# Kernel optimization log

Hardware: AMD Instinct MI355X
Metric: run time of the kernel (lower is better)

Reference implementation:

```python
import jax, jax.numpy as jnp
import numpy as np

_SAMPLING_EPS = 1e-5


def setup_inputs() -> dict:
    key = jax.random.key(0)
    k1, k2, k3, k4, k5 = jax.random.split(key, 5)
    B, V = 128, 128000
    logits = jax.random.normal(k1, (B, V), dtype=jnp.float32)
    temperature = jax.random.uniform(k2, (B,), dtype=jnp.float32)  # some rows < eps -> greedy
    top_k = jax.random.randint(k3, (B,), 1, 64, dtype=jnp.int32)   # in [1, 63]
    top_p = jax.random.uniform(k4, (B,), dtype=jnp.float32, minval=0.05, maxval=1.0)
    noise_u = jax.random.uniform(k5, (B, V), dtype=jnp.float32, minval=1e-10, maxval=1.0)
    return {"logits": logits, "temperature": temperature, "top_k": top_k,
            "top_p": top_p, "noise_u": noise_u, "max_num_logprobs": 5}


def _apply_top_k_top_p(logits, k, p):
    # Faithful to vLLM: ascending sort, top-k threshold mask, top-p cumsum mask, scatter back.
    B, V = logits.shape
    order = jnp.argsort(logits, axis=-1)                       # ascending, [B, V]
    logits_sort = jnp.take_along_axis(logits, order, axis=-1)
    neg_inf = jnp.float32(-jnp.inf)
    # top-k: pivot value at position V - k; everything strictly below it -> -inf
    pivot_idx = (V - k.astype(jnp.int32))[:, None]             # [B, 1]
    pivot = jnp.take_along_axis(logits_sort, pivot_idx, axis=-1)
    logits_sort = jnp.where(logits_sort < pivot, neg_inf, logits_sort)
    # top-p: softmax over sorted logits, cumsum, drop prefix with mass <= 1 - p (keep last)
    probs_sort = jax.nn.softmax(logits_sort, axis=-1)
    probs_sum = jnp.cumsum(probs_sort, axis=-1)
    top_p_mask = probs_sum <= (1.0 - p)[:, None]
    top_p_mask = top_p_mask.at[:, -1].set(False)
    logits_sort = jnp.where(top_p_mask, neg_inf, logits_sort)
    # scatter back to original vocab order
    rows = jnp.arange(B)[:, None]
    return jnp.zeros_like(logits).at[rows, order].set(logits_sort)


def reference(logits, temperature, top_k, top_p, noise_u, max_num_logprobs):
    # temperature scaling (temp < eps means greedy; divide by 1.0 instead)
    temp = jnp.where(temperature < _SAMPLING_EPS, 1.0, temperature)
    logits = logits.astype(jnp.float32) / temp[:, None]
    # top-k / top-p filtering
    logits = _apply_top_k_top_p(logits, top_k, top_p)
    # probabilities and sampling
    probs = jax.nn.softmax(logits, axis=-1)
    greedy = jnp.argmax(probs, axis=-1)
    q = -jnp.log(noise_u)                                      # Exp(1) noise (q.exponential_())
    random = jnp.argmax(probs / q, axis=-1)
    sampled = jnp.where(temperature < _SAMPLING_EPS, greedy, random).astype(jnp.int32)
    # top-k logprobs
    logprobs = jax.nn.log_softmax(logits, axis=-1)
    topk_logprobs, topk_indices = jax.lax.top_k(logprobs, max_num_logprobs)
    return sampled, topk_indices.astype(jnp.int32), topk_logprobs
```

## Files before the change

### kernel.cpp

```cpp
#include <hip/hip_runtime.h>
#include <math.h>
#include <stdint.h>

#define BT     256
#define TOPC   64
#define CAP    2048
#define WT     512
#define TILE   (BT * 8)
#define NCH    8
#define NC     (NCH * TOPC)

__device__ __forceinline__ unsigned f2ord(float f) {
    unsigned u = __float_as_uint(f);
    return u ^ ((u & 0x80000000u) ? 0xFFFFFFFFu : 0x80000000u);
}
__device__ __forceinline__ float ord2f(unsigned k) {
    unsigned u = (k & 0x80000000u) ? (k ^ 0x80000000u) : (k ^ 0xFFFFFFFFu);
    return __uint_as_float(u);
}

__device__ unsigned radix_select_compact4(uint2* s_buf, uint2* s_keep,
                                          unsigned (*s_hist)[16], unsigned* p_cnt2,
                                          unsigned n, int tid, int wid)
{
    unsigned prefix = 0u;
    int remaining = TOPC;
    for (int shift = 28; shift >= 0; shift -= 4) {
        if (tid < 64) ((unsigned*)s_hist)[tid] = 0u;
        __syncthreads();
        for (unsigned i = (unsigned)tid; i < n; i += BT) {
            unsigned k = s_buf[i].x;
            bool ing = (shift == 28) || ((k >> (shift + 4)) == (prefix >> (shift + 4)));
            if (ing) atomicAdd(&s_hist[wid][(k >> shift) & 15u], 1u);
        }
        __syncthreads();
        int cum = 0; int b = 0; unsigned hb = 0u;
        for (int bb = 15; bb >= 0; --bb) {
            unsigned h = s_hist[0][bb] + s_hist[1][bb] + s_hist[2][bb] + s_hist[3][bb];
            cum += (int)h;
            if (cum >= remaining) { b = bb; hb = h; break; }
        }
        remaining -= (cum - (int)hb);
        prefix |= ((unsigned)b) << shift;
        __syncthreads();
    }
    if (tid == 0) *p_cnt2 = 0u;
    __syncthreads();
    for (unsigned i = (unsigned)tid; i < n; i += BT) {
        uint2 c = s_buf[i];
        if (c.x > prefix) s_keep[atomicAdd(p_cnt2, 1u)] = c;
    }
    __syncthreads();
    for (unsigned i = (unsigned)tid; i < n; i += BT) {
        uint2 c = s_buf[i];
        if (c.x == prefix) {
            unsigned pos = atomicAdd(p_cnt2, 1u);
            if (pos < TOPC) s_keep[pos] = c;
        }
    }
    __syncthreads();
    return prefix;
}

__global__ __launch_bounds__(BT) void phase1_topk_chunks(
    const float* __restrict__ logits, uint2* __restrict__ cand,
    int V, int chunk_len, int nchunk)
{
    __shared__ uint2    s_buf[CAP];
    __shared__ uint2    s_keep[TOPC];
    __shared__ unsigned s_hist[4][16];
    __shared__ unsigned s_cnt, s_cnt2, s_ovf;

    const int row   = blockIdx.y;
    const int chunk = blockIdx.x;
    const int tid   = threadIdx.x;
    const int wid   = tid >> 6;
    const int lane  = tid & 63;
    const int c0    = chunk * chunk_len;
    int c1 = c0 + chunk_len; if (c1 > V) c1 = V;
    const float* rowp = logits + (size_t)row * (size_t)V;

    if (tid == 0) { s_cnt = 0u; s_ovf = 0u; }
    __syncthreads();

    const int slice_len = chunk_len >> 2;
    const int s0 = c0 + wid * slice_len;
    int s_end = s0 + slice_len; if (s_end > c1) s_end = c1;

    unsigned k0[8], k1[8];
    const int  b0  = s0 + lane * 8,  b1 = s0 + WT + lane * 8;
    const bool vv0 = (b0 < s_end),   vv1 = (b1 < s_end);
    if (vv0) {
        float4 a = *(const float4*)(rowp + b0);
        float4 b = *(const float4*)(rowp + b0 + 4);
        k0[0] = f2ord(a.x); k0[1] = f2ord(a.y); k0[2] = f2ord(a.z); k0[3] = f2ord(a.w);
        k0[4] = f2ord(b.x); k0[5] = f2ord(b.y); k0[6] = f2ord(b.z); k0[7] = f2ord(b.w);
    } else {
        #pragma unroll
        for (int j = 0; j < 8; ++j) k0[j] = 0u;
    }
    if (vv1) {
        float4 a = *(const float4*)(rowp + b1);
        float4 b = *(const float4*)(rowp + b1 + 4);
        k1[0] = f2ord(a.x); k1[1] = f2ord(a.y); k1[2] = f2ord(a.z); k1[3] = f2ord(a.w);
        k1[4] = f2ord(b.x); k1[5] = f2ord(b.y); k1[6] = f2ord(b.z); k1[7] = f2ord(b.w);
    } else {
        #pragma unroll
        for (int j = 0; j < 8; ++j) k1[j] = 0u;
    }

    float4 A0 = {}, B0 = {}, A1 = {}, B1 = {};
    bool v0 = false, v1 = false;
    const int t2 = s0 + 2 * WT, t3 = s0 + 3 * WT;
    if (t2 < s_end) {
        int bs = t2 + lane * 8;
        if (bs < s_end) { A0 = *(const float4*)(rowp + bs);
                          B0 = *(const float4*)(rowp + bs + 4); v0 = true; }
    }
    if (t3 < s_end) {
        int bs = t3 + lane * 8;
        if (bs < s_end) { A1 = *(const float4*)(rowp + bs);
                          B1 = *(const float4*)(rowp + bs + 4); v1 = true; }
    }

    unsigned lo = 0u, hi = 0xFFFFu;
    while (lo < hi) {
        unsigned mid = (lo + hi + 1u) >> 1;
        unsigned t = mid << 16;
        int cnt = 0;
        #pragma unroll
        for (int j = 0; j < 8; ++j) {
            cnt += __popcll(__ballot(k0[j] >= t));
            cnt += __popcll(__ballot(k1[j] >= t));
        }
        if (cnt >= TOPC) lo = mid; else hi = mid - 1u;
    }
    const unsigned thr = lo << 16;

    auto append8 = [&](const unsigned* k, int base, bool valid) {
        unsigned pm = 0u; unsigned np = 0u;
        if (valid) {
            #pragma unroll
            for (int j = 0; j < 8; ++j)
                if (k[j] >= thr) { pm |= (1u << j); ++np; }
        }
        if (np) {
            unsigned pos = atomicAdd(&s_cnt, np);
            #pragma unroll
            for (int j = 0; j < 8; ++j)
                if (pm & (1u << j)) {
                    if (pos < CAP) s_buf[pos] = make_uint2(k[j], (unsigned)(base + j));
                    ++pos;
                }
        }
    };

    append8(k0, b0, vv0);
    append8(k1, b1, vv1);

    for (int t = t2; t < s_end; t += WT) {
        float4 A2 = {}, B2 = {}; bool v2 = false;
        int tn = t + 2 * WT;
        if (tn < s_end) {
            int bs = tn + lane * 8;
            if (bs < s_end) { A2 = *(const float4*)(rowp + bs);
                              B2 = *(const float4*)(rowp + bs + 4); v2 = true; }
        }
        if (v0) {
            unsigned k[8];
            k[0] = f2ord(A0.x); k[1] = f2ord(A0.y); k[2] = f2ord(A0.z); k[3] = f2ord(A0.w);
            k[4] = f2ord(B0.x); k[5] = f2ord(B0.y); k[6] = f2ord(B0.z); k[7] = f2ord(B0.w);
            append8(k, t + lane * 8, true);
        }
        A0 = A1; B0 = B1; v0 = v1;
        A1 = A2; B1 = B2; v1 = v2;
    }

    __syncthreads();
    unsigned n = s_cnt;

    if (n > CAP) {
        unsigned vst = radix_select_compact4(s_buf, s_keep, s_hist, &s_cnt2,
                                             CAP, tid, wid);
        if (tid == 0) { s_cnt = 0u; s_ovf = 0u; }
        __syncthreads();
        for (int t = c0; t < c1; t += TILE) {
            int bs = t + tid * 8;
            unsigned k[8]; bool v = (bs < c1);
            if (v) {
                float4 a = *(const float4*)(rowp + bs);
                float4 b = *(const float4*)(rowp + bs + 4);
                k[0] = f2ord(a.x); k[1] = f2ord(a.y); k[2] = f2ord(a.z); k[3] = f2ord(a.w);
                k[4] = f2ord(b.x); k[5] = f2ord(b.y); k[6] = f2ord(b.z); k[7] = f2ord(b.w);
            } else {
                #pragma unroll
                for (int j = 0; j < 8; ++j) k[j] = 0u;
            }
            unsigned pm = 0u; int np = 0;
            if (v) {
                #pragma unroll
                for (int j = 0; j < 8; ++j)
                    if (k[j] >= vst) { pm |= (1u << j); ++np; }
            }
            for (;;) {
                if (np) {
                    unsigned pos = atomicAdd(&s_cnt, (unsigned)np);
                    unsigned rem = 0u; int nr = 0;
                    #pragma unroll
                    for (int j = 0; j < 8; ++j) {
                        if (pm & (1u << j)) {
                            if (pos < CAP) s_buf[pos] = make_uint2(k[j], (unsigned)(bs + j));
                            else { rem |= (1u << j); ++nr; }
                            ++pos;
                        }
                    }
                    if (nr) s_ovf = 1u;
                    pm = rem; np = nr;
                }
                __syncthreads();
                unsigned ovf = s_ovf;
                __syncthreads();
                if (!ovf) break;
                unsigned nn = s_cnt; if (nn > CAP) nn = CAP;
                unsigned v2s = radix_select_compact4(s_buf, s_keep, s_hist, &s_cnt2,
                                                     nn, tid, wid);
                if (tid < TOPC) s_buf[tid] = s_keep[tid];
                if (tid == 0) { s_cnt = TOPC; s_ovf = 0u; }
                __syncthreads();
                unsigned rem = 0u; int nr = 0;
                #pragma unroll
                for (int j = 0; j < 8; ++j)
                    if ((pm & (1u << j)) && k[j] > v2s) { rem |= (1u << j); ++nr; }
                pm = rem; np = nr;
            }
        }
        n = s_cnt; if (n > CAP) n = CAP;
    }

    if (n < TOPC) {
        for (unsigned i = n + (unsigned)tid; i < TOPC; i += BT)
            s_buf[i] = make_uint2(0u, (unsigned)((c0 < V) ? c0 : 0));
        n = TOPC;
        __syncthreads();
    }

    radix_select_compact4(s_buf, s_keep, s_hist, &s_cnt2, n, tid, wid);
    if (tid < TOPC)
        cand[((size_t)row * (unsigned)nchunk + (unsigned)chunk) * TOPC + tid] = s_keep[tid];
}

__global__ __launch_bounds__(BT) void phase2_sample(
    const uint2* __restrict__ cand,
    const float* __restrict__ temperature,
    const int*   __restrict__ top_k,
    const float* __restrict__ top_p,
    const float* __restrict__ noise_u,
    float* __restrict__ out,
    int B, int V, int M, int nc)
{
    __shared__ uint2    s_buf[NC];
    __shared__ uint2    s_keep[TOPC];
    __shared__ unsigned s_hist[4][16];
    __shared__ unsigned s_cnt2;
    __shared__ float    sval[TOPC], se[TOPC], sq[TOPC];
    __shared__ int      sidx[TOPC];

    const int r   = blockIdx.x;
    const int tid = threadIdx.x;
    const int wid = tid >> 6;

    for (int i = tid; i < nc; i += BT)
        s_buf[i] = cand[(size_t)r * nc + i];
    __syncthreads();
    radix_select_compact4(s_buf, s_keep, s_hist, &s_cnt2, (unsigned)nc, tid, wid);

    for (int kk = 2; kk <= TOPC; kk <<= 1) {
        for (int j = kk >> 1; j > 0; j >>= 1) {
            if (tid < TOPC / 2) {
                int i0 = ((tid & ~(j - 1)) << 1) | (tid & (j - 1));
                int i1 = i0 | j;
                bool up = ((i0 & kk) == 0);
                uint2 A = s_keep[i0], Bv = s_keep[i1];
                bool gt = (A.x < Bv.x) || (A.x == Bv.x && A.y > Bv.y);
                if (gt == up) { s_keep[i0] = Bv; s_keep[i1] = A; }
            }
            __syncthreads();
        }
    }

    float temp_orig = temperature[r];
    float temp = (temp_orig < 1e-5f) ? 1.0f : temp_orig;

    if (tid < TOPC) {
        unsigned k = s_keep[tid].x;
        int id = (int)s_keep[tid].y;
        sval[tid] = ord2f(k) / temp;
        sidx[tid] = id;
        float u = noise_u[(size_t)r * (size_t)V + id];
        sq[tid] = -logf(u);
    }
    __syncthreads();
    if (tid < TOPC) se[tid] = expf(sval[tid] - sval[0]);
    __syncthreads();

    if (tid == 0) {
        int k = top_k[r];
        if (k < 1) k = 1; if (k > TOPC) k = TOPC;
        float p = top_p[r];

        float pivot = sval[k - 1];
        int m = k;
        while (m < TOPC && sval[m] >= pivot) ++m;

        float sum = 0.f;
        for (int i = 0; i < m; ++i) sum += se[i];

        float thr1 = 1.0f - p;
        float S = 0.f;
        int f = 1;
        for (int i = m - 1; i >= 1; --i) {
            S += se[i] / sum;
            if (S > thr1) { f = i + 1; break; }
        }

        float sum2 = 0.f;
        for (int i = 0; i < f; ++i) sum2 += se[i];

        int greedy = sidx[0];
        float best = -1.f; int bidx = 0x7fffffff;
        for (int i = 0; i < f; ++i) {
            float ratio = (se[i] / sum2) / sq[i];
            if (ratio > best || (ratio == best && sidx[i] < bidx)) {
                best = ratio; bidx = sidx[i];
            }
        }
        int sampled = (temp_orig < 1e-5f) ? greedy : bidx;

        float lse = logf(sum2);
        out[r] = (float)sampled;
        float* oidx = out + B + (size_t)r * M;
        float* olp  = out + B + (size_t)B * M + (size_t)r * M;
        int produced = 0;
        for (int i = 0; i < f && produced < M; ++i, ++produced) {
            oidx[produced] = (float)sidx[i];
            olp[produced]  = (sval[i] - sval[0]) - lse;
        }
        int v = 0;
        while (produced < M) {
            bool used = false;
            for (int i = 0; i < f; ++i) if (sidx[i] == v) { used = true; break; }
            if (!used) { oidx[produced] = (float)v; olp[produced] = -3.0e38f; ++produced; }
            ++v;
        }
    }
}

extern "C" void kernel_launch(void* const* d_in, const int* in_sizes, int n_in,
                              void* d_out, int out_size, void* d_ws, size_t ws_size,
                              hipStream_t stream)
{
    const float* logits      = (const float*)d_in[0];
    const float* temperature = (const float*)d_in[1];
    const int*   top_k       = (const int*)d_in[2];
    const float* top_p       = (const float*)d_in[3];
    const float* noise_u     = (const float*)d_in[4];

    const int B = in_sizes[1];
    const int V = in_sizes[0] / B;
    const int M = (out_size / B - 1) / 2;

    uint2* cand = (uint2*)d_ws;

    int chunk_len = (((V + NCH - 1) / NCH) + 31) & ~31;

    dim3 g1(NCH, B);
    phase1_topk_chunks<<<g1, BT, 0, stream>>>(logits, cand, V, chunk_len, NCH);
    phase2_sample<<<B, BT, 0, stream>>>(cand, temperature, top_k, top_p, noise_u,
                                        (float*)d_out, B, V, M, NC);
}
```

Baseline: 181.3 us.

## Double phase-1 chunks per row and prefetch eight tiles ahead

Phase 1 now uses 16 chunks per row when the workspace is large enough, falling back to 8 otherwise, so the grid has twice as many blocks. Phase 2 sizes its candidate buffer to the new maximum. Phase 1 also issues loads for eight tiles up front instead of a rolling two-tile prefetch, putting more memory requests in flight per wave. The cost is twice as many candidates to merge in phase 2 and higher register pressure in phase 1.

```diff
diff --git a/kernel.cpp b/kernel.cpp
--- a/kernel.cpp
+++ b/kernel.cpp
@@ -7,8 +7,9 @@
 #define CAP    2048
 #define WT     512
 #define TILE   (BT * 8)
-#define NCH    8
-#define NC     (NCH * TOPC)
+#define NCH_HI 16
+#define NCH_LO 8
+#define NC_MAX (NCH_HI * TOPC)
 
 __device__ __forceinline__ unsigned f2ord(float f) {
     unsigned u = __float_as_uint(f);
@@ -87,41 +88,39 @@
     const int s0 = c0 + wid * slice_len;
     int s_end = s0 + slice_len; if (s_end > c1) s_end = c1;
 
+    const int  tb0 = s0 + 0 * WT + lane * 8, tb1 = s0 + 1 * WT + lane * 8;
+    const int  tb2 = s0 + 2 * WT + lane * 8, tb3 = s0 + 3 * WT + lane * 8;
+    const int  tb4 = s0 + 4 * WT + lane * 8, tb5 = s0 + 5 * WT + lane * 8;
+    const int  tb6 = s0 + 6 * WT + lane * 8, tb7 = s0 + 7 * WT + lane * 8;
+    const bool vt0 = tb0 < s_end, vt1 = tb1 < s_end, vt2 = tb2 < s_end,
+               vt3 = tb3 < s_end, vt4 = tb4 < s_end, vt5 = tb5 < s_end,
+               vt6 = tb6 < s_end, vt7 = tb7 < s_end;
+
+    float4 a0 = {}, b0 = {}, a1 = {}, b1 = {};
+    float4 a2 = {}, b2 = {}, a3 = {}, b3 = {};
+    if (vt0) { a0 = *(const float4*)(rowp + tb0); b0 = *(const float4*)(rowp + tb0 + 4); }
+    if (vt1) { a1 = *(const float4*)(rowp + tb1); b1 = *(const float4*)(rowp + tb1 + 4); }
+    if (vt2) { a2 = *(const float4*)(rowp + tb2); b2 = *(const float4*)(rowp + tb2 + 4); }
+    if (vt3) { a3 = *(const float4*)(rowp + tb3); b3 = *(const float4*)(rowp + tb3 + 4); }
+
     unsigned k0[8], k1[8];
-    const int  b0  = s0 + lane * 8,  b1 = s0 + WT + lane * 8;
-    const bool vv0 = (b0 < s_end),   vv1 = (b1 < s_end);
-    if (vv0) {
-        float4 a = *(const float4*)(rowp + b0);
-        float4 b = *(const float4*)(rowp + b0 + 4);
-        k0[0] = f2ord(a.x); k0[1] = f2ord(a.y); k0[2] = f2ord(a.z); k0[3] = f2ord(a.w);
-        k0[4] = f2ord(b.x); k0[5] = f2ord(b.y); k0[6] = f2ord(b.z); k0[7] = f2ord(b.w);
+    if (vt0) {
+        k0[0] = f2ord(a0.x); k0[1] = f2ord(a0.y); k0[2] = f2ord(a0.z); k0[3] = f2ord(a0.w);
+        k0[4] = f2ord(b0.x); k0[5] = f2ord(b0.y); k0[6] = f2ord(b0.z); k0[7] = f2ord(b0.w);
     } else {
         #pragma unroll
         for (int j = 0; j < 8; ++j) k0[j] = 0u;
     }
-    if (vv1) {
-        float4 a = *(const float4*)(rowp + b1);
-        float4 b = *(const float4*)(rowp + b1 + 4);
-        k1[0] = f2ord(a.x); k1[1] = f2ord(a.y); k1[2] = f2ord(a.z); k1[3] = f2ord(a.w);
-        k1[4] = f2ord(b.x); k1[5] = f2ord(b.y); k1[6] = f2ord(b.z); k1[7] = f2ord(b.w);
+    if (vt1) {
+        k1[0] = f2ord(a1.x); k1[1] = f2ord(a1.y); k1[2] = f2ord(a1.z); k1[3] = f2ord(a1.w);
+        k1[4] = f2ord(b1.x); k1[5] = f2ord(b1.y); k1[6] = f2ord(b1.z); k1[7] = f2ord(b1.w);
     } else {
         #pragma unroll
         for (int j = 0; j < 8; ++j) k1[j] = 0u;
     }
 
-    float4 A0 = {}, B0 = {}, A1 = {}, B1 = {};
-    bool v0 = false, v1 = false;
-    const int t2 = s0 + 2 * WT, t3 = s0 + 3 * WT;
-    if (t2 < s_end) {
-        int bs = t2 + lane * 8;
-        if (bs < s_end) { A0 = *(const float4*)(rowp + bs);
-                          B0 = *(const float4*)(rowp + bs + 4); v0 = true; }
-    }
-    if (t3 < s_end) {
-        int bs = t3 + lane * 8;
-        if (bs < s_end) { A1 = *(const float4*)(rowp + bs);
-                          B1 = *(const float4*)(rowp + bs + 4); v1 = true; }
-    }
+    if (vt4) { a0 = *(const float4*)(rowp + tb4); b0 = *(const float4*)(rowp + tb4 + 4); }
+    if (vt5) { a1 = *(const float4*)(rowp + tb5); b1 = *(const float4*)(rowp + tb5 + 4); }
 
     unsigned lo = 0u, hi = 0xFFFFu;
     while (lo < hi) {
@@ -154,26 +153,44 @@
                 }
         }
     };
-
-    append8(k0, b0, vv0);
-    append8(k1, b1, vv1);
-
-    for (int t = t2; t < s_end; t += WT) {
-        float4 A2 = {}, B2 = {}; bool v2 = false;
-        int tn = t + 2 * WT;
-        if (tn < s_end) {
-            int bs = tn + lane * 8;
-            if (bs < s_end) { A2 = *(const float4*)(rowp + bs);
-                              B2 = *(const float4*)(rowp + bs + 4); v2 = true; }
-        }
-        if (v0) {
-            unsigned k[8];
-            k[0] = f2ord(A0.x); k[1] = f2ord(A0.y); k[2] = f2ord(A0.z); k[3] = f2ord(A0.w);
-            k[4] = f2ord(B0.x); k[5] = f2ord(B0.y); k[6] = f2ord(B0.z); k[7] = f2ord(B0.w);
-            append8(k, t + lane * 8, true);
-        }
-        A0 = A1; B0 = B1; v0 = v1;
-        A1 = A2; B1 = B2; v1 = v2;
+    auto conv8 = [&](unsigned* k, const float4& a, const float4& b, bool valid) {
+        if (valid) {
+            k[0] = f2ord(a.x); k[1] = f2ord(a.y); k[2] = f2ord(a.z); k[3] = f2ord(a.w);
+            k[4] = f2ord(b.x); k[5] = f2ord(b.y); k[6] = f2ord(b.z); k[7] = f2ord(b.w);
+        } else {
+            #pragma unroll
+            for (int j = 0; j < 8; ++j) k[j] = 0u;
+        }
+    };
+
+    append8(k0, tb0, vt0);
+    append8(k1, tb1, vt1);
+
+    {
+        unsigned kk[8];
+        conv8(kk, a2, b2, vt2);
+        if (vt6) { a2 = *(const float4*)(rowp + tb6); b2 = *(const float4*)(rowp + tb6 + 4); }
+        append8(kk, tb2, vt2);
+    }
+    {
+        unsigned kk[8];
+        conv8(kk, a3, b3, vt3);
+        if (vt7) { a3 = *(const float4*)(rowp + tb7); b3 = *(const float4*)(rowp + tb7 + 4); }
+        append8(kk, tb3, vt3);
+    }
+    {   unsigned kk[8]; conv8(kk, a0, b0, vt4); append8(kk, tb4, vt4); }
+    {   unsigned kk[8]; conv8(kk, a1, b1, vt5); append8(kk, tb5, vt5); }
+    {   unsigned kk[8]; conv8(kk, a2, b2, vt6); append8(kk, tb6, vt6); }
+    {   unsigned kk[8]; conv8(kk, a3, b3, vt7); append8(kk, tb7, vt7); }
+
+    for (int t = s0 + 8 * WT; t < s_end; t += WT) {
+        int bs = t + lane * 8;
+        bool v = bs < s_end;
+        float4 aa = {}, bb = {};
+        if (v) { aa = *(const float4*)(rowp + bs); bb = *(const float4*)(rowp + bs + 4); }
+        unsigned kk[8];
+        conv8(kk, aa, bb, v);
+        append8(kk, bs, v);
     }
 
     __syncthreads();
@@ -258,7 +275,7 @@
     float* __restrict__ out,
     int B, int V, int M, int nc)
 {
-    __shared__ uint2    s_buf[NC];
+    __shared__ uint2    s_buf[NC_MAX];
     __shared__ uint2    s_keep[TOPC];
     __shared__ unsigned s_hist[4][16];
     __shared__ unsigned s_cnt2;
@@ -369,12 +386,15 @@
     const int V = in_sizes[0] / B;
     const int M = (out_size / B - 1) / 2;
 
+    const size_t cand16 = (size_t)B * NCH_HI * TOPC * sizeof(uint2);
+    const int nch = (ws_size >= cand16) ? NCH_HI : NCH_LO;
+
     uint2* cand = (uint2*)d_ws;
 
-    int chunk_len = (((V + NCH - 1) / NCH) + 31) & ~31;
-
-    dim3 g1(NCH, B);
-    phase1_topk_chunks<<<g1, BT, 0, stream>>>(logits, cand, V, chunk_len, NCH);
+    int chunk_len = (((V + nch - 1) / nch) + 31) & ~31;
+
+    dim3 g1(nch, B);
+    phase1_topk_chunks<<<g1, BT, 0, stream>>>(logits, cand, V, chunk_len, nch);
     phase2_sample<<<B, BT, 0, stream>>>(cand, temperature, top_k, top_p, noise_u,
-                                        (float*)d_out, B, V, M, NC);
-}
+                                        (float*)d_out, B, V, M, nch * TOPC);
+}
```

New measurement: 192.4 us. +6.1%, slower.

## Replace per-chunk top-k with global row threshold, grid-wide filter, and single select

Applied to the files above, without the earlier changes.

The old per-chunk top-64 selection (8 chunks per row, then a merge in phase 2) is replaced by three kernels. The first estimates a per-row threshold from the first 4096 logits, which is guaranteed to keep at least 64 elements. The second is a grid-stride filter over all tiles that appends survivors to a global per-row buffer using wave ballots and one atomic per wave. The third selects the top 64 from the survivors, falling back to a full-row rescan if the buffer overflows. This spreads the streaming filter across all CUs with cheap wave-level compaction, at the cost of an extra launch and global atomics and scattered survivor writes.

```diff
diff --git a/kernel.cpp b/kernel.cpp
--- a/kernel.cpp
+++ b/kernel.cpp
@@ -2,13 +2,11 @@
 #include <math.h>
 #include <stdint.h>
 
-#define BT     256
-#define TOPC   64
-#define CAP    2048
-#define WT     512
-#define TILE   (BT * 8)
-#define NCH    8
-#define NC     (NCH * TOPC)
+#define BT    256
+#define TOPC  64
+#define SAMPN 4096
+#define FT    512
+#define CAP2  4096
 
 __device__ __forceinline__ unsigned f2ord(float f) {
     unsigned u = __float_as_uint(f);
@@ -62,145 +60,153 @@
     return prefix;
 }
 
-__global__ __launch_bounds__(BT) void phase1_topk_chunks(
-    const float* __restrict__ logits, uint2* __restrict__ cand,
-    int V, int chunk_len, int nchunk)
-{
-    __shared__ uint2    s_buf[CAP];
-    __shared__ uint2    s_keep[TOPC];
-    __shared__ unsigned s_hist[4][16];
-    __shared__ unsigned s_cnt, s_cnt2, s_ovf;
-
-    const int row   = blockIdx.y;
-    const int chunk = blockIdx.x;
-    const int tid   = threadIdx.x;
-    const int wid   = tid >> 6;
-    const int lane  = tid & 63;
-    const int c0    = chunk * chunk_len;
-    int c1 = c0 + chunk_len; if (c1 > V) c1 = V;
-    const float* rowp = logits + (size_t)row * (size_t)V;
-
-    if (tid == 0) { s_cnt = 0u; s_ovf = 0u; }
-    __syncthreads();
-
-    const int slice_len = chunk_len >> 2;
-    const int s0 = c0 + wid * slice_len;
-    int s_end = s0 + slice_len; if (s_end > c1) s_end = c1;
-
-    unsigned k0[8], k1[8];
-    const int  b0  = s0 + lane * 8,  b1 = s0 + WT + lane * 8;
-    const bool vv0 = (b0 < s_end),   vv1 = (b1 < s_end);
-    if (vv0) {
-        float4 a = *(const float4*)(rowp + b0);
-        float4 b = *(const float4*)(rowp + b0 + 4);
-        k0[0] = f2ord(a.x); k0[1] = f2ord(a.y); k0[2] = f2ord(a.z); k0[3] = f2ord(a.w);
-        k0[4] = f2ord(b.x); k0[5] = f2ord(b.y); k0[6] = f2ord(b.z); k0[7] = f2ord(b.w);
-    } else {
-        #pragma unroll
-        for (int j = 0; j < 8; ++j) k0[j] = 0u;
-    }
-    if (vv1) {
-        float4 a = *(const float4*)(rowp + b1);
-        float4 b = *(const float4*)(rowp + b1 + 4);
-        k1[0] = f2ord(a.x); k1[1] = f2ord(a.y); k1[2] = f2ord(a.z); k1[3] = f2ord(a.w);
-        k1[4] = f2ord(b.x); k1[5] = f2ord(b.y); k1[6] = f2ord(b.z); k1[7] = f2ord(b.w);
-    } else {
-        #pragma unroll
-        for (int j = 0; j < 8; ++j) k1[j] = 0u;
-    }
-
-    float4 A0 = {}, B0 = {}, A1 = {}, B1 = {};
-    bool v0 = false, v1 = false;
-    const int t2 = s0 + 2 * WT, t3 = s0 + 3 * WT;
-    if (t2 < s_end) {
-        int bs = t2 + lane * 8;
-        if (bs < s_end) { A0 = *(const float4*)(rowp + bs);
-                          B0 = *(const float4*)(rowp + bs + 4); v0 = true; }
-    }
-    if (t3 < s_end) {
-        int bs = t3 + lane * 8;
-        if (bs < s_end) { A1 = *(const float4*)(rowp + bs);
-                          B1 = *(const float4*)(rowp + bs + 4); v1 = true; }
+__global__ __launch_bounds__(64) void row_thresh(
+    const float* __restrict__ logits, unsigned* __restrict__ thr,
+    unsigned* __restrict__ counts, int V)
+{
+    const int r    = blockIdx.x;
+    const int lane = threadIdx.x;
+    const float* rowp = logits + (size_t)r * (size_t)V;
+
+    unsigned kr[64];
+    #pragma unroll
+    for (int g = 0; g < 8; ++g) {
+        int c0 = g * 512 + lane * 8;
+        if (c0 < V) {
+            float4 a = *(const float4*)(rowp + c0);
+            float4 b = *(const float4*)(rowp + c0 + 4);
+            kr[g * 8 + 0] = f2ord(a.x); kr[g * 8 + 1] = f2ord(a.y);
+            kr[g * 8 + 2] = f2ord(a.z); kr[g * 8 + 3] = f2ord(a.w);
+            kr[g * 8 + 4] = f2ord(b.x); kr[g * 8 + 5] = f2ord(b.y);
+            kr[g * 8 + 6] = f2ord(b.z); kr[g * 8 + 7] = f2ord(b.w);
+        } else {
+            #pragma unroll
+            for (int j = 0; j < 8; ++j) kr[g * 8 + j] = 0u;
+        }
     }
 
     unsigned lo = 0u, hi = 0xFFFFu;
     while (lo < hi) {
         unsigned mid = (lo + hi + 1u) >> 1;
         unsigned t = mid << 16;
-        int cnt = 0;
+        int c = 0;
+        #pragma unroll
+        for (int j = 0; j < 64; ++j) c += __popcll(__ballot(kr[j] >= t));
+        if (c >= TOPC) lo = mid; else hi = mid - 1u;
+    }
+    if (lane == 0) { thr[r] = lo << 16; counts[r] = 0u; }
+}
+
+__global__ __launch_bounds__(BT) void filter_pass(
+    const float* __restrict__ logits, const unsigned* __restrict__ thr,
+    unsigned* __restrict__ counts, uint2* __restrict__ surv,
+    int B, int V, int tpr, int cap2)
+{
+    const int tid  = threadIdx.x;
+    const int wid  = tid >> 6;
+    const int lane = tid & 63;
+    const unsigned long long ltm = (1ull << lane) - 1ull;
+    const int nw = gridDim.x * (BT / 64);
+    const int ntiles = B * tpr;
+
+    for (int tw = blockIdx.x * (BT / 64) + wid; tw < ntiles; tw += nw) {
+        const int t    = __builtin_amdgcn_readfirstlane(tw);
+        const int row  = t / tpr;
+        const int col0 = (t - row * tpr) * FT + lane * 8;
+        const bool v   = col0 < V;
+        const float* rowp = logits + (size_t)row * (size_t)V;
+
+        unsigned k[8];
+        if (v) {
+            float4 a = *(const float4*)(rowp + col0);
+            float4 b = *(const float4*)(rowp + col0 + 4);
+            k[0] = f2ord(a.x); k[1] = f2ord(a.y); k[2] = f2ord(a.z); k[3] = f2ord(a.w);
+            k[4] = f2ord(b.x); k[5] = f2ord(b.y); k[6] = f2ord(b.z); k[7] = f2ord(b.w);
+        } else {
+            #pragma unroll
+            for (int j = 0; j < 8; ++j) k[j] = 0u;
+        }
+
+        const unsigned tr = thr[row];
+        unsigned long long m[8]; unsigned c[8]; unsigned tot = 0u;
         #pragma unroll
         for (int j = 0; j < 8; ++j) {
-            cnt += __popcll(__ballot(k0[j] >= t));
-            cnt += __popcll(__ballot(k1[j] >= t));
-        }
-        if (cnt >= TOPC) lo = mid; else hi = mid - 1u;
-    }
-    const unsigned thr = lo << 16;
-
-    auto append8 = [&](const unsigned* k, int base, bool valid) {
-        unsigned pm = 0u; unsigned np = 0u;
-        if (valid) {
+            m[j] = __ballot(v && (k[j] >= tr));
+            c[j] = tot;
+            tot += (unsigned)__popcll(m[j]);
+        }
+        unsigned base = 0u;
+        if (lane == 0 && tot) base = atomicAdd(&counts[row], tot);
+        base = __shfl(base, 0);
+        if (tot) {
             #pragma unroll
-            for (int j = 0; j < 8; ++j)
-                if (k[j] >= thr) { pm |= (1u << j); ++np; }
-        }
-        if (np) {
-            unsigned pos = atomicAdd(&s_cnt, np);
-            #pragma unroll
-            for (int j = 0; j < 8; ++j)
-                if (pm & (1u << j)) {
-                    if (pos < CAP) s_buf[pos] = make_uint2(k[j], (unsigned)(base + j));
-                    ++pos;
+            for (int j = 0; j < 8; ++j) {
+                if (v && (k[j] >= tr)) {
+                    unsigned pos = base + c[j] + (unsigned)__popcll(m[j] & ltm);
+                    if (pos < (unsigned)cap2)
+                        surv[(size_t)row * (unsigned)cap2 + pos] =
+                            make_uint2(k[j], (unsigned)(col0 + j));
                 }
-        }
-    };
-
-    append8(k0, b0, vv0);
-    append8(k1, b1, vv1);
-
-    for (int t = t2; t < s_end; t += WT) {
-        float4 A2 = {}, B2 = {}; bool v2 = false;
-        int tn = t + 2 * WT;
-        if (tn < s_end) {
-            int bs = tn + lane * 8;
-            if (bs < s_end) { A2 = *(const float4*)(rowp + bs);
-                              B2 = *(const float4*)(rowp + bs + 4); v2 = true; }
-        }
-        if (v0) {
-            unsigned k[8];
-            k[0] = f2ord(A0.x); k[1] = f2ord(A0.y); k[2] = f2ord(A0.z); k[3] = f2ord(A0.w);
-            k[4] = f2ord(B0.x); k[5] = f2ord(B0.y); k[6] = f2ord(B0.z); k[7] = f2ord(B0.w);
-            append8(k, t + lane * 8, true);
-        }
-        A0 = A1; B0 = B1; v0 = v1;
-        A1 = A2; B1 = B2; v1 = v2;
-    }
-
-    __syncthreads();
-    unsigned n = s_cnt;
-
-    if (n > CAP) {
-        unsigned vst = radix_select_compact4(s_buf, s_keep, s_hist, &s_cnt2,
-                                             CAP, tid, wid);
+            }
+        }
+    }
+}
+
+__global__ __launch_bounds__(BT) void phase2_sample(
+    const uint2* __restrict__ surv, const unsigned* __restrict__ counts,
+    const unsigned* __restrict__ thr, const float* __restrict__ logits,
+    const float* __restrict__ temperature,
+    const int*   __restrict__ top_k,
+    const float* __restrict__ top_p,
+    const float* __restrict__ noise_u,
+    float* __restrict__ out,
+    int B, int V, int M, int cap2)
+{
+    __shared__ uint2    s_buf[CAP2];
+    __shared__ uint2    s_keep[TOPC];
+    __shared__ unsigned s_hist[4][16];
+    __shared__ unsigned s_cnt, s_cnt2, s_ovf;
+    __shared__ float    sval[TOPC], se[TOPC], sq[TOPC];
+    __shared__ int      sidx[TOPC];
+
+    const int r   = blockIdx.x;
+    const int tid = threadIdx.x;
+    const int wid = tid >> 6;
+
+    const unsigned n_true = counts[r];
+    unsigned n;
+
+    if (n_true <= (unsigned)cap2) {
+        n = n_true;
+        for (unsigned i = (unsigned)tid; i < n; i += BT)
+            s_buf[i] = surv[(size_t)r * (unsigned)cap2 + i];
+        __syncthreads();
+    } else {
+        const float* rowp = logits + (size_t)r * (size_t)V;
         if (tid == 0) { s_cnt = 0u; s_ovf = 0u; }
         __syncthreads();
-        for (int t = c0; t < c1; t += TILE) {
+        unsigned vst = thr[r];
+        bool strict = false;
+        for (int t = 0; t < V; t += BT * 8) {
             int bs = t + tid * 8;
-            unsigned k[8]; bool v = (bs < c1);
+            bool v = bs < V;
+            unsigned kk[8];
             if (v) {
                 float4 a = *(const float4*)(rowp + bs);
                 float4 b = *(const float4*)(rowp + bs + 4);
-                k[0] = f2ord(a.x); k[1] = f2ord(a.y); k[2] = f2ord(a.z); k[3] = f2ord(a.w);
-                k[4] = f2ord(b.x); k[5] = f2ord(b.y); k[6] = f2ord(b.z); k[7] = f2ord(b.w);
+                kk[0] = f2ord(a.x); kk[1] = f2ord(a.y); kk[2] = f2ord(a.z); kk[3] = f2ord(a.w);
+                kk[4] = f2ord(b.x); kk[5] = f2ord(b.y); kk[6] = f2ord(b.z); kk[7] = f2ord(b.w);
             } else {
                 #pragma unroll
-                for (int j = 0; j < 8; ++j) k[j] = 0u;
+                for (int j = 0; j < 8; ++j) kk[j] = 0u;
             }
             unsigned pm = 0u; int np = 0;
             if (v) {
                 #pragma unroll
-                for (int j = 0; j < 8; ++j)
-                    if (k[j] >= vst) { pm |= (1u << j); ++np; }
+                for (int j = 0; j < 8; ++j) {
+                    bool pa = strict ? (kk[j] > vst) : (kk[j] >= vst);
+                    if (pa) { pm |= (1u << j); ++np; }
+                }
             }
             for (;;) {
                 if (np) {
@@ -209,7 +215,7 @@
                     #pragma unroll
                     for (int j = 0; j < 8; ++j) {
                         if (pm & (1u << j)) {
-                            if (pos < CAP) s_buf[pos] = make_uint2(k[j], (unsigned)(bs + j));
+                            if (pos < CAP2) s_buf[pos] = make_uint2(kk[j], (unsigned)(bs + j));
                             else { rem |= (1u << j); ++nr; }
                             ++pos;
                         }
@@ -221,7 +227,7 @@
                 unsigned ovf = s_ovf;
                 __syncthreads();
                 if (!ovf) break;
-                unsigned nn = s_cnt; if (nn > CAP) nn = CAP;
+                unsigned nn = s_cnt; if (nn > CAP2) nn = CAP2;
                 unsigned v2s = radix_select_compact4(s_buf, s_keep, s_hist, &s_cnt2,
                                                      nn, tid, wid);
                 if (tid < TOPC) s_buf[tid] = s_keep[tid];
@@ -230,49 +236,22 @@
                 unsigned rem = 0u; int nr = 0;
                 #pragma unroll
                 for (int j = 0; j < 8; ++j)
-                    if ((pm & (1u << j)) && k[j] > v2s) { rem |= (1u << j); ++nr; }
+                    if ((pm & (1u << j)) && kk[j] > v2s) { rem |= (1u << j); ++nr; }
                 pm = rem; np = nr;
-            }
-        }
-        n = s_cnt; if (n > CAP) n = CAP;
+                vst = v2s; strict = true;
+            }
+        }
+        n = s_cnt; if (n > CAP2) n = CAP2;
     }
 
     if (n < TOPC) {
         for (unsigned i = n + (unsigned)tid; i < TOPC; i += BT)
-            s_buf[i] = make_uint2(0u, (unsigned)((c0 < V) ? c0 : 0));
+            s_buf[i] = make_uint2(0u, 0u);
         n = TOPC;
         __syncthreads();
     }
 
     radix_select_compact4(s_buf, s_keep, s_hist, &s_cnt2, n, tid, wid);
-    if (tid < TOPC)
-        cand[((size_t)row * (unsigned)nchunk + (unsigned)chunk) * TOPC + tid] = s_keep[tid];
-}
-
-__global__ __launch_bounds__(BT) void phase2_sample(
-    const uint2* __restrict__ cand,
-    const float* __restrict__ temperature,
-    const int*   __restrict__ top_k,
-    const float* __restrict__ top_p,
-    const float* __restrict__ noise_u,
-    float* __restrict__ out,
-    int B, int V, int M, int nc)
-{
-    __shared__ uint2    s_buf[NC];
-    __shared__ uint2    s_keep[TOPC];
-    __shared__ unsigned s_hist[4][16];
-    __shared__ unsigned s_cnt2;
-    __shared__ float    sval[TOPC], se[TOPC], sq[TOPC];
-    __shared__ int      sidx[TOPC];
-
-    const int r   = blockIdx.x;
-    const int tid = threadIdx.x;
-    const int wid = tid >> 6;
-
-    for (int i = tid; i < nc; i += BT)
-        s_buf[i] = cand[(size_t)r * nc + i];
-    __syncthreads();
-    radix_select_compact4(s_buf, s_keep, s_hist, &s_cnt2, (unsigned)nc, tid, wid);
 
     for (int kk = 2; kk <= TOPC; kk <<= 1) {
         for (int j = kk >> 1; j > 0; j >>= 1) {
@@ -369,12 +348,27 @@
     const int V = in_sizes[0] / B;
     const int M = (out_size / B - 1) / 2;
 
-    uint2* cand = (uint2*)d_ws;
-
-    int chunk_len = (((V + NCH - 1) / NCH) + 31) & ~31;
-
-    dim3 g1(NCH, B);
-    phase1_topk_chunks<<<g1, BT, 0, stream>>>(logits, cand, V, chunk_len, NCH);
-    phase2_sample<<<B, BT, 0, stream>>>(cand, temperature, top_k, top_p, noise_u,
-                                        (float*)d_out, B, V, M, NC);
-}
+    unsigned* thr    = (unsigned*)d_ws;
+    unsigned* counts = thr + B;
+    size_t off = (((size_t)2 * B * sizeof(unsigned)) + 7) & ~(size_t)7;
+    uint2* surv = (uint2*)((char*)d_ws + off);
+
+    int cap2 = CAP2;
+    if (ws_size > off) {
+        size_t avail = (ws_size - off) / ((size_t)B * sizeof(uint2));
+        if (avail < (size_t)cap2) cap2 = (int)avail;
+    }
+    if (cap2 < TOPC) cap2 = TOPC;
+
+    const int tpr = (V + FT - 1) / FT;
+    const int ntiles = B * tpr;
+    int fblocks = (ntiles + 3) / 4;
+    if (fblocks > 2048) fblocks = 2048;
+
+    row_thresh<<<B, 64, 0, stream>>>(logits, thr, counts, V);
+    filter_pass<<<fblocks, BT, 0, stream>>>(logits, thr, counts, surv,
+                                            B, V, tpr, cap2);
+    phase2_sample<<<B, BT, 0, stream>>>(surv, counts, thr, logits,
+                                        temperature, top_k, top_p, noise_u,
+                                        (float*)d_out, B, V, M, cap2);
+}
```

Measured after the change: 365.1 us. 101% more time.
